# Kernel optimization log

Measured on AMD Instinct MI355X. Metric: run time of the kernel, lower is better.

The kernel has to match this reference:

```python
import jax, jax.numpy as jnp
import numpy as np

N = 20000
NEG_SLOPE = 0.2


def gatv2_layer(x, src, dst, edge_attr, Wl, bl, Wr, br, We, att, bias, H, C):
    """PyG GATv2Conv: add self-loops (edge_attr fill='mean'), gather-score-softmax-aggregate."""
    n = x.shape[0]
    E = src.shape[0]
    # --- add self loops, self-loop edge_attr = mean of incoming edge_attr per node ---
    ea_sum = jax.ops.segment_sum(edge_attr, dst, num_segments=n)
    deg = jax.ops.segment_sum(jnp.ones((E, 1), x.dtype), dst, num_segments=n)
    ea_loop = ea_sum / jnp.maximum(deg, 1.0)
    loop = jnp.arange(n)
    src_a = jnp.concatenate([src, loop])
    dst_a = jnp.concatenate([dst, loop])
    ea = jnp.concatenate([edge_attr, ea_loop], axis=0)
    # --- linear projections ---
    xl = (x @ Wl + bl).reshape(n, H, C)   # source-side features
    xr = (x @ Wr + br).reshape(n, H, C)   # target-side features
    e = (ea @ We).reshape(-1, H, C)       # edge features
    # --- per-edge GATv2 attention score ---
    m = xl[src_a] + xr[dst_a] + e                          # [E', H, C]
    s = jnp.sum(jax.nn.leaky_relu(m, NEG_SLOPE) * att, -1)  # [E', H]
    # --- softmax over incoming edges of each target node ---
    smax = jax.ops.segment_max(s, dst_a, num_segments=n)
    ex = jnp.exp(s - smax[dst_a])
    denom = jax.ops.segment_sum(ex, dst_a, num_segments=n)
    alpha = ex / (denom[dst_a] + 1e-16)                    # [E', H]
    # --- aggregate messages (alpha * x_l[src]) ---
    out = jax.ops.segment_sum(alpha[..., None] * xl[src_a], dst_a, num_segments=n)
    return out.reshape(n, H * C) + bias


def setup_inputs() -> dict:
    key = jax.random.key(0)
    ks = jax.random.split(key, 20)
    F, HID, H1, A = 128, 32, 8, 128
    E = 640000
    d = {}
    d["x"] = jax.random.normal(ks[0], (N, F), jnp.float32)
    d["edge_index"] = jax.random.randint(ks[1], (2, E), 0, N, jnp.int32).astype(jnp.int64)
    d["edge_attr"] = jax.random.normal(ks[2], (E, 1), jnp.float32)
    # layer 1 params (in=F, out=HID, heads=H1)
    d["W1l"] = jax.random.normal(ks[3], (F, H1 * HID), jnp.float32) * 0.05
    d["b1l"] = jnp.zeros((H1 * HID,), jnp.float32)
    d["W1r"] = jax.random.normal(ks[4], (F, H1 * HID), jnp.float32) * 0.05
    d["b1r"] = jnp.zeros((H1 * HID,), jnp.float32)
    d["We1"] = jax.random.normal(ks[5], (1, H1 * HID), jnp.float32) * 0.05
    d["att1"] = jax.random.normal(ks[6], (H1, HID), jnp.float32) * 0.05
    d["bias1"] = jnp.zeros((H1 * HID,), jnp.float32)
    # layer 2 params (in=H1*HID, out=A, heads=1)
    d["W2l"] = jax.random.normal(ks[7], (H1 * HID, A), jnp.float32) * 0.05
    d["b2l"] = jnp.zeros((A,), jnp.float32)
    d["W2r"] = jax.random.normal(ks[8], (H1 * HID, A), jnp.float32) * 0.05
    d["b2r"] = jnp.zeros((A,), jnp.float32)
    d["We2"] = jax.random.normal(ks[9], (1, A), jnp.float32) * 0.05
    d["att2"] = jax.random.normal(ks[10], (1, A), jnp.float32) * 0.05
    d["bias2"] = jnp.zeros((A,), jnp.float32)
    d["alpha"] = jnp.array(0.0, jnp.float32)
    return d


def reference(x, edge_index, edge_attr, W1l, b1l, W1r, b1r, We1, att1, bias1,
              W2l, b2l, W2r, b2r, We2, att2, bias2, alpha):
    src, dst = edge_index[0], edge_index[1]
    h = jax.nn.relu(gatv2_layer(x, src, dst, edge_attr, W1l, b1l, W1r, b1r,
                                We1, att1, bias1, H=8, C=32))
    h = jax.nn.relu(gatv2_layer(h, src, dst, edge_attr, W2l, b2l, W2r, b2r,
                                We2, att2, bias2, H=1, C=128))
    pooled = jnp.mean(h, axis=0, keepdims=True)  # global_mean_pool, single graph -> [1, A]
    return jax.nn.softmax(pooled, axis=1), jax.nn.sigmoid(alpha)
```

## Files before the change

### kernel.cpp

```cpp
#include <hip/hip_runtime.h>
#include <math.h>

#define NEG_SLOPE 0.2f
#define LOG2E 1.4426950408889634f

typedef __attribute__((ext_vector_type(8))) short short8;
typedef __attribute__((ext_vector_type(4))) float f32x4;
typedef __attribute__((ext_vector_type(2))) float v2f;

__device__ __forceinline__ int imin(int a, int b) { return a < b ? a : b; }

__device__ __forceinline__ unsigned int f2bf(float f) {
    unsigned int u = __float_as_uint(f);
    return (u + 0x7fffu + ((u >> 16) & 1u)) >> 16;
}
__device__ __forceinline__ float fast_exp2(float x) {
#if __has_builtin(__builtin_amdgcn_exp2f)
    return __builtin_amdgcn_exp2f(x);
#else
    return exp2f(x);
#endif
}
__device__ __forceinline__ unsigned char f2fp8(float v) {
    return (unsigned char)(__builtin_amdgcn_cvt_pk_fp8_f32(v, v, 0, false) & 0xff);
}
template <int CTRL>
__device__ __forceinline__ float dpp_add(float v) {
    int t = __builtin_amdgcn_update_dpp(0, __float_as_int(v), CTRL, 0xF, 0xF, true);
    return v + __int_as_float(t);
}
__device__ __forceinline__ v2f pk_fma(v2f a, v2f b, v2f c) {
    v2f d;
    asm("v_pk_fma_f32 %0, %1, %2, %3" : "=v"(d) : "v"(a), "v"(b), "v"(c));
    return d;
}
__device__ __forceinline__ v2f pk_add(v2f a, v2f b) {
    v2f d;
    asm("v_pk_add_f32 %0, %1, %2" : "=v"(d) : "v"(a), "v"(b));
    return d;
}

__global__ void fused_prep(const int* __restrict__ ei, const float* __restrict__ ea,
                           unsigned long long* __restrict__ hist, int E,
                           const float* __restrict__ x, unsigned short* __restrict__ xb, int nF4,
                           const float* __restrict__ W1l, const float* __restrict__ W1r,
                           const float* __restrict__ W2l, const float* __restrict__ W2r,
                           const float* __restrict__ b1l, const float* __restrict__ b1r,
                           const float* __restrict__ b2l, const float* __restrict__ b2r,
                           unsigned short* __restrict__ Wt1, unsigned short* __restrict__ Wt2,
                           float* __restrict__ b1cat, float* __restrict__ b2cat,
                           int F, int HC1, int HC2) {
    int i = blockIdx.x * blockDim.x + threadIdx.x;
    if (i < E) {
        int d = ei[E + i];
        long long fx = (long long)__float2int_rn(ea[i] * 65536.0f);
        unsigned long long v = ((unsigned long long)fx << 32) | 1ull;
        atomicAdd(&hist[(size_t)d * 8], v);
        return;
    }
    int j = i - E;
    if (j < nF4) {
        float4 v = ((const float4*)x)[j];
        uint2 r;
        r.x = f2bf(v.x) | (f2bf(v.y) << 16);
        r.y = f2bf(v.z) | (f2bf(v.w) << 16);
        ((uint2*)xb)[j] = r;
        return;
    }
    int k = j - nF4;
    int S1 = F * HC1, S2 = HC1 * HC2;
    if (k < S1) {
        int kk = k / HC1, nn = k - kk * HC1;
        Wt1[(size_t)nn * F + kk] = (unsigned short)f2bf(W1l[k]);
    } else if (k < 2 * S1) {
        int m = k - S1;
        int kk = m / HC1, nn = m - kk * HC1;
        Wt1[(size_t)(HC1 + nn) * F + kk] = (unsigned short)f2bf(W1r[m]);
    } else if (k < 2 * S1 + S2) {
        int m = k - 2 * S1;
        int kk = m / HC2, nn = m - kk * HC2;
        Wt2[(size_t)nn * HC1 + kk] = (unsigned short)f2bf(W2l[m]);
    } else if (k < 2 * S1 + 2 * S2) {
        int m = k - 2 * S1 - S2;
        int kk = m / HC2, nn = m - kk * HC2;
        Wt2[(size_t)(HC2 + nn) * HC1 + kk] = (unsigned short)f2bf(W2r[m]);
    } else if (k < 2 * S1 + 2 * S2 + 2 * HC1) {
        int m = k - 2 * S1 - 2 * S2;
        b1cat[m] = (m < HC1) ? b1l[m] : b1r[m - HC1];
    } else if (k < 2 * S1 + 2 * S2 + 2 * HC1 + 2 * HC2) {
        int m = k - 2 * S1 - 2 * S2 - 2 * HC1;
        b2cat[m] = (m < HC2) ? b2l[m] : b2r[m - HC2];
    }
}

__global__ void scan_a(const unsigned long long* __restrict__ hist, int* __restrict__ bsum, int n) {
    __shared__ int wred[4];
    int base = blockIdx.x * 1024;
    int tid = threadIdx.x;
    int s = 0;
#pragma unroll
    for (int k = 0; k < 4; ++k) {
        int i = base + tid + k * 256;
        if (i < n) s += (int)(hist[(size_t)i * 8] & 0xffffffffull);
    }
#pragma unroll
    for (int off = 32; off > 0; off >>= 1) s += __shfl_xor(s, off, 64);
    if ((tid & 63) == 0) wred[tid >> 6] = s;
    __syncthreads();
    if (tid == 0) bsum[blockIdx.x] = wred[0] + wred[1] + wred[2] + wred[3];
}

__global__ void scan_c(const unsigned long long* __restrict__ hist,
                       const int* __restrict__ bsum, int* __restrict__ row_ptr,
                       int* __restrict__ wptr_pad, float* __restrict__ ea_loop,
                       int n, int B) {
    __shared__ int wtot[4];
    __shared__ int sh_base;
    int tid = threadIdx.x;
    int wid = tid >> 6, lane = tid & 63;
    int i0 = blockIdx.x * 1024 + tid * 4;
    int dcnt[4]; float esum[4];
#pragma unroll
    for (int k = 0; k < 4; ++k) {
        if (i0 + k < n) {
            unsigned long long h = hist[(size_t)(i0 + k) * 8];
            dcnt[k] = (int)(h & 0xffffffffull);
            esum[k] = (float)((int)(h >> 32)) * (1.0f / 65536.0f);
        } else { dcnt[k] = 0; esum[k] = 0.0f; }
    }
    int tsum = dcnt[0] + dcnt[1] + dcnt[2] + dcnt[3];
    int s = tsum;
#pragma unroll
    for (int off = 1; off < 64; off <<= 1) {
        int t = __shfl_up(s, off, 64);
        if (lane >= off) s += t;
    }
    if (lane == 63) wtot[wid] = s;
    if (tid < 64) {
        int v   = (tid < B) ? bsum[tid] : 0;
        int pre = (tid < (int)blockIdx.x) ? v : 0;
        int tot = v;
#pragma unroll
        for (int off = 32; off > 0; off >>= 1) {
            pre += __shfl_xor(pre, off, 64);
            tot += __shfl_xor(tot, off, 64);
        }
        if (tid == 0) {
            sh_base = pre;
            if (blockIdx.x == 0) row_ptr[n] = tot;
        }
    }
    __syncthreads();
    int wpre = 0;
#pragma unroll
    for (int k = 0; k < 4; ++k) if (k < wid) wpre += wtot[k];
    int pre = sh_base + wpre + (s - tsum);
    if (i0 < n) {
        int4 e;
        e.x = pre;
        e.y = pre + dcnt[0];
        e.z = e.y + dcnt[1];
        e.w = e.z + dcnt[2];
        *(int4*)(row_ptr + i0) = e;
        int ev[4] = { e.x, e.y, e.z, e.w };
        float4 el;
        el.x = esum[0] / fmaxf((float)dcnt[0], 1.0f);
        el.y = esum[1] / fmaxf((float)dcnt[1], 1.0f);
        el.z = esum[2] / fmaxf((float)dcnt[2], 1.0f);
        el.w = esum[3] / fmaxf((float)dcnt[3], 1.0f);
        *(float4*)(ea_loop + i0) = el;
#pragma unroll
        for (int k = 0; k < 4; ++k) wptr_pad[(size_t)(i0 + k) * 16] = ev[k];
    }
}

__global__ void edge_scatter(const int* __restrict__ ei, const float* __restrict__ ea,
                             int* __restrict__ wptr_pad, int2* __restrict__ spk, int E) {
    int e = blockIdx.x * blockDim.x + threadIdx.x;
    if (e < E) {
        int d = ei[E + e];
        int pos = atomicAdd(&wptr_pad[(size_t)d * 16], 1);
        spk[pos] = make_int2(ei[e], __float_as_int(ea[e]));
    }
}

template <bool OUT_FP8>
__global__ void __launch_bounds__(256)
gemm_bf16(const unsigned short* __restrict__ A, const unsigned short* __restrict__ Bt,
          const float* __restrict__ bias, void* __restrict__ Cv,
          int M, int N, int K) {
    __shared__ __attribute__((aligned(16))) unsigned short As[64 * 40];
    __shared__ __attribute__((aligned(16))) unsigned short Bs[64 * 40];
    int tid  = threadIdx.x;
    int wave = tid >> 6, lane = tid & 63;
    int m0 = blockIdx.x * 64, n0 = blockIdx.y * 64;
    int row = tid >> 2, kg = (tid & 3) * 8;

    f32x4 acc[4] = {};
    for (int kk = 0; kk < K; kk += 32) {
        int gm = m0 + row;
        uint4 av;
        if (gm < M) av = *(const uint4*)(A + (size_t)gm * K + kk + kg);
        else        av = make_uint4(0, 0, 0, 0);
        *(uint4*)&As[row * 40 + kg] = av;
        uint4 bv = *(const uint4*)(Bt + (size_t)(n0 + row) * K + kk + kg);
        *(uint4*)&Bs[row * 40 + kg] = bv;
        __syncthreads();
        short8 a = *(const short8*)&As[(wave * 16 + (lane & 15)) * 40 + (lane >> 4) * 8];
#pragma unroll
        for (int g = 0; g < 4; ++g) {
            short8 b = *(const short8*)&Bs[(g * 16 + (lane & 15)) * 40 + (lane >> 4) * 8];
            acc[g] = __builtin_amdgcn_mfma_f32_16x16x32_bf16(a, b, acc[g], 0, 0, 0);
        }
        __syncthreads();
    }
#pragma unroll
    for (int g = 0; g < 4; ++g) {
        int col = n0 + g * 16 + (lane & 15);
        float bs = bias[col];
#pragma unroll
        for (int r = 0; r < 4; ++r) {
            int grow = m0 + wave * 16 + (lane >> 4) * 4 + r;
            if (grow < M) {
                float val = acc[g][r] + bs;
                if constexpr (OUT_FP8) {
                    ((unsigned char*)Cv)[(size_t)grow * N + col] = f2fp8(val);
                } else {
                    ((unsigned short*)Cv)[(size_t)grow * N + col] = (unsigned short)f2bf(val);
                }
            }
        }
    }
}

template <int NV>
__device__ __forceinline__ void unp1(unsigned int u, v2f* xf) {
    xf[0] = __builtin_amdgcn_cvt_pk_f32_fp8(u, false);
    if constexpr (NV == 4) xf[1] = __builtin_amdgcn_cvt_pk_f32_fp8(u, true);
}
template <int G>
__device__ __forceinline__ float grp_reduce(float vs) {
    vs = dpp_add<0xB1>(vs);
    if constexpr (G >= 4)  vs = dpp_add<0x4E>(vs);
    if constexpr (G >= 8)  vs = dpp_add<0x141>(vs);
    if constexpr (G >= 16) vs = dpp_add<0x140>(vs);
    if constexpr (G >= 32) {
        int t = __builtin_amdgcn_ds_swizzle(__float_as_int(vs), 0x401F);
        vs += __int_as_float(t);
    }
    if constexpr (G >= 64) vs += __shfl_xor(vs, 32, 64);
    return vs;
}

template <int HC, int STRIDE, int C, int OUT_MODE>
__global__ void __launch_bounds__(256)
gat_agg(const unsigned char* __restrict__ xlr,
        const float* __restrict__ We, const float* __restrict__ att,
        const float* __restrict__ bias,
        const int* __restrict__ row_ptr, const int2* __restrict__ spk,
        const float* __restrict__ ea_loop,
        void* __restrict__ out, int n) {
    constexpr int NV = HC / 64;
    constexpr int NG = (NV + 1) / 2;
    constexpr int G  = C / NV;
    constexpr int SHIFT = (STRIDE == 512) ? 9 : 8;
    constexpr float K23 = 2.0f / 3.0f;
    __shared__ float red[4][128];
    int wave = threadIdx.x >> 6;
    int lane = threadIdx.x & 63;
    int node = blockIdx.x * 4 + wave;
    bool active = node < n;
    if (OUT_MODE == 0 && !active) return;
    unsigned int lo = (unsigned int)lane * NV;

    float vout[NV];
#pragma unroll
    for (int j = 0; j < NV; ++j) vout[j] = 0.0f;

    if (active) {
        auto ldd = [&](unsigned int off) -> unsigned int {
            if constexpr (NV == 4) return *(const unsigned int*)(xlr + off);
            else                   return (unsigned int)(*(const unsigned short*)(xlr + off));
        };
        auto gat = [&](int s) -> unsigned int {
            return ldd(((unsigned int)s << SHIFT) + lo);
        };
        auto W = [&](int2 s) -> float { return __int_as_float(s.y); };

        v2f xr2[NG], We2[NG], att62[NG], o2[NG];
        {
            v2f tmp[NG];
            unp1<NV>(ldd(((unsigned int)node << SHIFT) + HC + lo), tmp);
#pragma unroll
            for (int g = 0; g < NG; ++g) xr2[g] = tmp[g];
        }
#pragma unroll
        for (int g = 0; g < NG; ++g) {
            We2[g]   = *(const v2f*)(We  + lo + 2 * g);
            v2f a    = *(const v2f*)(att + lo + 2 * g);
            att62[g] = a * (0.6f * LOG2E);
            o2[g]    = v2f{0.0f, 0.0f};
        }
        float l = 0.0f;

        int start = __builtin_amdgcn_readfirstlane(row_ptr[node]);
        int end   = __builtin_amdgcn_readfirstlane(row_ptr[node + 1]);
        float ea_l = ea_loop[node];

        auto process = [&](unsigned int du, float w) {
            v2f xf[NG];
            unp1<NV>(du, xf);
            v2f w2 = {w, w};
            v2f vs6 = {0.0f, 0.0f};
            float vs4 = 0.0f;
#pragma unroll
            for (int g = 0; g < NG; ++g) {
                v2f t  = pk_fma(w2, We2[g], xr2[g]);
                v2f mm = pk_add(xf[g], t);
                vs6 = pk_fma(att62[g], mm, vs6);
                vs4 = fmaf(fabsf(mm.x), att62[g].x, vs4);
                vs4 = fmaf(fabsf(mm.y), att62[g].y, vs4);
            }
            float vs = fmaf(K23, vs4, vs6.x + vs6.y);
            vs = grp_reduce<G>(vs);
            float pr = fast_exp2(vs);
            l += pr;
            v2f pr2 = {pr, pr};
#pragma unroll
            for (int g = 0; g < NG; ++g) o2[g] = pk_fma(xf[g], pr2, o2[g]);
        };

        process(ldd(((unsigned int)node << SHIFT) + lo), ea_l);

        int cnt = end - start;
        const int2* q = spk + start;

        if (cnt >= 6) {
            int2 t;
            t = q[0]; unsigned int g0 = gat(t.x); float w0 = W(t);
            t = q[1]; unsigned int g1 = gat(t.x); float w1 = W(t);
            t = q[2]; unsigned int g2 = gat(t.x); float w2 = W(t);
            t = q[3]; unsigned int g3 = gat(t.x); float w3 = W(t);
            t = q[4]; unsigned int g4 = gat(t.x); float w4 = W(t);
            t = q[5]; unsigned int g5 = gat(t.x); float w5 = W(t);
            int p = 0;
            for (; p + 12 <= cnt; p += 6) {
                process(g0, w0); t = q[p + 6];  g0 = gat(t.x); w0 = W(t);
                process(g1, w1); t = q[p + 7];  g1 = gat(t.x); w1 = W(t);
                process(g2, w2); t = q[p + 8];  g2 = gat(t.x); w2 = W(t);
                process(g3, w3); t = q[p + 9];  g3 = gat(t.x); w3 = W(t);
                process(g4, w4); t = q[p + 10]; g4 = gat(t.x); w4 = W(t);
                process(g5, w5); t = q[p + 11]; g5 = gat(t.x); w5 = W(t);
            }
            process(g0, w0); process(g1, w1); process(g2, w2);
            process(g3, w3); process(g4, w4); process(g5, w5);
            for (int k = p + 6; k < cnt; ++k) {
                t = q[k];
                process(gat(t.x), W(t));
            }
        } else {
            for (int k = 0; k < cnt; ++k) {
                int2 t = q[k];
                process(gat(t.x), W(t));
            }
        }

        float inv = 1.0f / (l + 1e-16f);
#pragma unroll
        for (int g = 0; g < NG; ++g) {
            v2f b = *(const v2f*)(bias + lo + 2 * g);
            vout[2 * g]     = fmaxf(o2[g].x * inv + b.x, 0.0f);
            vout[2 * g + 1] = fmaxf(o2[g].y * inv + b.y, 0.0f);
        }
        if constexpr (OUT_MODE == 0) {
            unsigned short* op = (unsigned short*)out + (size_t)node * HC + lo;
            if constexpr (NV == 4) {
                uint2 t;
                t.x = f2bf(vout[0]) | (f2bf(vout[1]) << 16);
                t.y = f2bf(vout[2]) | (f2bf(vout[3]) << 16);
                *(uint2*)op = t;
            } else {
                *(unsigned int*)op = f2bf(vout[0]) | (f2bf(vout[1]) << 16);
            }
        }
    }

    if constexpr (OUT_MODE == 1) {
#pragma unroll
        for (int j = 0; j < NV; ++j) red[wave][lo + j] = vout[j];
        __syncthreads();
        if (wave == 0) {
            int c = lane;
            float a = red[0][c] + red[1][c] + red[2][c] + red[3][c];
            float b = red[0][c + 64] + red[1][c + 64] + red[2][c + 64] + red[3][c + 64];
            float* pacc = (float*)out + (size_t)(blockIdx.x & 255) * 128;
            atomicAdd(&pacc[c], a);
            atomicAdd(&pacc[c + 64], b);
        }
    }
}

__global__ void __launch_bounds__(1024)
pool_final(const float* __restrict__ partial, int nb,
           const float* __restrict__ alpha_in,
           float* __restrict__ out, int n) {
    __shared__ float acc[8][128];
    __shared__ float red[4];
    int t = threadIdx.x & 127;
    int g = threadIdx.x >> 7;
    float s = 0.0f;
    for (int b = g; b < nb; b += 8) s += partial[b * 128 + t];
    acc[g][t] = s;
    __syncthreads();
    if (threadIdx.x < 128) {
        float tot = 0.0f;
#pragma unroll
        for (int k = 0; k < 8; ++k) tot += acc[k][t];
        float mean = tot / (float)n;
        float mx = mean;
#pragma unroll
        for (int off = 32; off > 0; off >>= 1) mx = fmaxf(mx, __shfl_xor(mx, off, 64));
        if ((t & 63) == 0) red[t >> 6] = mx;
        __syncthreads();
        mx = fmaxf(red[0], red[1]);
        float ex = __expf(mean - mx);
        float sm = ex;
#pragma unroll
        for (int off = 32; off > 0; off >>= 1) sm += __shfl_xor(sm, off, 64);
        if ((t & 63) == 0) red[2 + (t >> 6)] = sm;
        __syncthreads();
        sm = red[2] + red[3];
        out[t] = ex / sm;
        if (t == 0) out[128] = 1.0f / (1.0f + __expf(-alpha_in[0]));
    }
}

extern "C" void kernel_launch(void* const* d_in, const int* in_sizes, int n_in,
                              void* d_out, int out_size, void* d_ws, size_t ws_size,
                              hipStream_t stream) {
    const float* x    = (const float*)d_in[0];
    const int*   ei   = (const int*)d_in[1];
    const float* ea   = (const float*)d_in[2];
    const float* W1l  = (const float*)d_in[3];
    const float* b1l  = (const float*)d_in[4];
    const float* W1r  = (const float*)d_in[5];
    const float* b1r  = (const float*)d_in[6];
    const float* We1  = (const float*)d_in[7];
    const float* att1 = (const float*)d_in[8];
    const float* bias1= (const float*)d_in[9];
    const float* W2l  = (const float*)d_in[10];
    const float* b2l  = (const float*)d_in[11];
    const float* W2r  = (const float*)d_in[12];
    const float* b2r  = (const float*)d_in[13];
    const float* We2  = (const float*)d_in[14];
    const float* att2 = (const float*)d_in[15];
    const float* bias2= (const float*)d_in[16];
    const float* alpha= (const float*)d_in[17];
    float* out = (float*)d_out;

    const int F = 128, HC1 = 256, HC2 = 128;
    const int n = in_sizes[0] / F;
    const int E = in_sizes[1] / 2;
    const int B = (n + 1023) / 1024;

    char* ws = (char*)d_ws;
    size_t off = 0;
    auto alloc = [&](size_t bytes) { size_t p = off; off += (bytes + 255) & ~(size_t)255; return p; };

    unsigned long long* hist = (unsigned long long*)(ws + alloc((size_t)n * 8 * 8));
    int*   row_ptr = (int*)  (ws + alloc((size_t)(n + 1) * 4));
    int*   wptr    = (int*)  (ws + alloc((size_t)n * 16 * 4));
    float* ea_loop = (float*)(ws + alloc((size_t)n * 4));
    int*   bsum    = (int*)  (ws + alloc(64 * 4));
    int2*  spk     = (int2*) (ws + alloc((size_t)E * 8));
    unsigned short* xb   = (unsigned short*)(ws + alloc((size_t)n * F * 2));
    unsigned short* Wt1  = (unsigned short*)(ws + alloc((size_t)F * (2 * HC1) * 2));
    unsigned short* Wt2  = (unsigned short*)(ws + alloc((size_t)HC1 * (2 * HC2) * 2));
    float* b1cat   = (float*)(ws + alloc((size_t)2 * HC1 * 4));
    float* b2cat   = (float*)(ws + alloc((size_t)2 * HC2 * 4));
    unsigned char* xlr1 = (unsigned char*)(ws + alloc((size_t)n * 2 * HC1));
    unsigned short* h1  = (unsigned short*)(ws + alloc((size_t)n * HC1 * 2));
    float* partial = (float*)(ws + alloc((size_t)256 * 128 * 4));
    unsigned char* xlr2 = xlr1;
    const int NB_SLOTS = 256;

    (void)hipMemsetAsync(hist, 0, (size_t)n * 8 * 8, stream);
    (void)hipMemsetAsync(partial, 0, (size_t)NB_SLOTS * 128 * 4, stream);

    int tb = 256;
    {
        int nF4  = n * F / 4;
        int WTOT = 2 * F * HC1 + 2 * HC1 * HC2 + 2 * HC1 + 2 * HC2;
        int total = E + nF4 + WTOT;
        fused_prep<<<(total + tb - 1) / tb, tb, 0, stream>>>(
            ei, ea, hist, E, x, xb, nF4,
            W1l, W1r, W2l, W2r, b1l, b1r, b2l, b2r,
            Wt1, Wt2, b1cat, b2cat, F, HC1, HC2);
    }
    scan_a<<<B, 256, 0, stream>>>(hist, bsum, n);
    scan_c<<<B, 256, 0, stream>>>(hist, bsum, row_ptr, wptr, ea_loop, n, B);
    edge_scatter<<<(E + tb - 1) / tb, tb, 0, stream>>>(ei, ea, wptr, spk, E);

    {
        dim3 grid((n + 63) / 64, (2 * HC1) / 64);
        gemm_bf16<true><<<grid, 256, 0, stream>>>(xb, Wt1, b1cat, xlr1, n, 2 * HC1, F);
    }
    gat_agg<256, 512, 32, 0><<<(n + 3) / 4, 256, 0, stream>>>(
        xlr1, We1, att1, bias1, row_ptr, spk, ea_loop, h1, n);

    {
        dim3 grid((n + 63) / 64, (2 * HC2) / 64);
        gemm_bf16<true><<<grid, 256, 0, stream>>>(h1, Wt2, b2cat, xlr2, n, 2 * HC2, HC1);
    }
    gat_agg<128, 256, 128, 1><<<(n + 3) / 4, 256, 0, stream>>>(
        xlr2, We2, att2, bias2, row_ptr, spk, ea_loop, partial, n);

    pool_final<<<1, 1024, 0, stream>>>(partial, NB_SLOTS, alpha, out, n);
}
```

Measured before the change: 276.5 us.

## Load edge list cooperatively per wave and broadcast via readlane with deeper prefetch

Each wave now loads up to 64 (src, weight) edge pairs in one coalesced vector load, one per lane. It then broadcasts each pair with readlane instead of issuing per-edge uniform loads. The gather pipeline changes from a rolling 6-deep prefetch to double-buffered batches of 8 outstanding neighbour-row gathers, and the self-row load is issued earlier. This is meant to cut scalar load latency on the edge list and keep more gathers in flight, at the cost of more registers and readlane overhead.

```diff
diff --git a/kernel.cpp b/kernel.cpp
--- a/kernel.cpp
+++ b/kernel.cpp
@@ -285,7 +285,16 @@
         auto gat = [&](int s) -> unsigned int {
             return ldd(((unsigned int)s << SHIFT) + lo);
         };
-        auto W = [&](int2 s) -> float { return __int_as_float(s.y); };
+
+        int start = __builtin_amdgcn_readfirstlane(row_ptr[node]);
+        int end   = __builtin_amdgcn_readfirstlane(row_ptr[node + 1]);
+        int cnt = end - start;
+
+        int2 pv;
+        if (cnt > 0) pv = spk[imin(start + lane, end - 1)];
+
+        unsigned int selfg = ldd(((unsigned int)node << SHIFT) + lo);
+        float ea_l = ea_loop[node];
 
         v2f xr2[NG], We2[NG], att62[NG], o2[NG];
         {
@@ -302,10 +311,6 @@
             o2[g]    = v2f{0.0f, 0.0f};
         }
         float l = 0.0f;
-
-        int start = __builtin_amdgcn_readfirstlane(row_ptr[node]);
-        int end   = __builtin_amdgcn_readfirstlane(row_ptr[node + 1]);
-        float ea_l = ea_loop[node];
 
         auto process = [&](unsigned int du, float w) {
             v2f xf[NG];
@@ -329,40 +334,56 @@
 #pragma unroll
             for (int g = 0; g < NG; ++g) o2[g] = pk_fma(xf[g], pr2, o2[g]);
         };
-
-        process(ldd(((unsigned int)node << SHIFT) + lo), ea_l);
-
-        int cnt = end - start;
-        const int2* q = spk + start;
-
-        if (cnt >= 6) {
-            int2 t;
-            t = q[0]; unsigned int g0 = gat(t.x); float w0 = W(t);
-            t = q[1]; unsigned int g1 = gat(t.x); float w1 = W(t);
-            t = q[2]; unsigned int g2 = gat(t.x); float w2 = W(t);
-            t = q[3]; unsigned int g3 = gat(t.x); float w3 = W(t);
-            t = q[4]; unsigned int g4 = gat(t.x); float w4 = W(t);
-            t = q[5]; unsigned int g5 = gat(t.x); float w5 = W(t);
-            int p = 0;
-            for (; p + 12 <= cnt; p += 6) {
-                process(g0, w0); t = q[p + 6];  g0 = gat(t.x); w0 = W(t);
-                process(g1, w1); t = q[p + 7];  g1 = gat(t.x); w1 = W(t);
-                process(g2, w2); t = q[p + 8];  g2 = gat(t.x); w2 = W(t);
-                process(g3, w3); t = q[p + 9];  g3 = gat(t.x); w3 = W(t);
-                process(g4, w4); t = q[p + 10]; g4 = gat(t.x); w4 = W(t);
-                process(g5, w5); t = q[p + 11]; g5 = gat(t.x); w5 = W(t);
+        auto RLs = [&](int k) -> int { return __builtin_amdgcn_readlane(pv.x, k); };
+        auto RLw = [&](int k) -> float { return __int_as_float(__builtin_amdgcn_readlane(pv.y, k)); };
+
+        process(selfg, ea_l);
+
+        int b0 = 0;
+        while (b0 < cnt) {
+            int rem = imin(64, cnt - b0);
+            int rc = rem - 1;
+            if (rem >= 8) {
+                unsigned int a0 = gat(RLs(0)), a1 = gat(RLs(1)), a2 = gat(RLs(2)), a3 = gat(RLs(3));
+                unsigned int a4 = gat(RLs(4)), a5 = gat(RLs(5)), a6 = gat(RLs(6)), a7 = gat(RLs(7));
+                float x0 = RLw(0), x1 = RLw(1), x2 = RLw(2), x3 = RLw(3);
+                float x4 = RLw(4), x5 = RLw(5), x6 = RLw(6), x7 = RLw(7);
+                int p = 0;
+                for (; p + 16 <= rem; p += 16) {
+                    unsigned int b0r = gat(RLs(p + 8)),  b1r = gat(RLs(p + 9));
+                    unsigned int b2r = gat(RLs(p + 10)), b3r = gat(RLs(p + 11));
+                    unsigned int b4r = gat(RLs(p + 12)), b5r = gat(RLs(p + 13));
+                    unsigned int b6r = gat(RLs(p + 14)), b7r = gat(RLs(p + 15));
+                    float y0 = RLw(p + 8),  y1 = RLw(p + 9),  y2 = RLw(p + 10), y3 = RLw(p + 11);
+                    float y4 = RLw(p + 12), y5 = RLw(p + 13), y6 = RLw(p + 14), y7 = RLw(p + 15);
+                    process(a0, x0); process(a1, x1); process(a2, x2); process(a3, x3);
+                    process(a4, x4); process(a5, x5); process(a6, x6); process(a7, x7);
+                    a0 = gat(RLs(imin(p + 16, rc))); a1 = gat(RLs(imin(p + 17, rc)));
+                    a2 = gat(RLs(imin(p + 18, rc))); a3 = gat(RLs(imin(p + 19, rc)));
+                    a4 = gat(RLs(imin(p + 20, rc))); a5 = gat(RLs(imin(p + 21, rc)));
+                    a6 = gat(RLs(imin(p + 22, rc))); a7 = gat(RLs(imin(p + 23, rc)));
+                    x0 = RLw(imin(p + 16, rc)); x1 = RLw(imin(p + 17, rc));
+                    x2 = RLw(imin(p + 18, rc)); x3 = RLw(imin(p + 19, rc));
+                    x4 = RLw(imin(p + 20, rc)); x5 = RLw(imin(p + 21, rc));
+                    x6 = RLw(imin(p + 22, rc)); x7 = RLw(imin(p + 23, rc));
+                    process(b0r, y0); process(b1r, y1); process(b2r, y2); process(b3r, y3);
+                    process(b4r, y4); process(b5r, y5); process(b6r, y6); process(b7r, y7);
+                }
+                int r = rem - p;
+                if (r > 0) process(a0, x0);
+                if (r > 1) process(a1, x1);
+                if (r > 2) process(a2, x2);
+                if (r > 3) process(a3, x3);
+                if (r > 4) process(a4, x4);
+                if (r > 5) process(a5, x5);
+                if (r > 6) process(a6, x6);
+                if (r > 7) process(a7, x7);
+                for (int k = p + 8; k < rem; ++k) process(gat(RLs(k)), RLw(k));
+            } else {
+                for (int k = 0; k < rem; ++k) process(gat(RLs(k)), RLw(k));
             }
-            process(g0, w0); process(g1, w1); process(g2, w2);
-            process(g3, w3); process(g4, w4); process(g5, w5);
-            for (int k = p + 6; k < cnt; ++k) {
-                t = q[k];
-                process(gat(t.x), W(t));
-            }
-        } else {
-            for (int k = 0; k < cnt; ++k) {
-                int2 t = q[k];
-                process(gat(t.x), W(t));
-            }
+            b0 += 64;
+            if (b0 < cnt) pv = spk[imin(start + b0 + lane, end - 1)];
         }
 
         float inv = 1.0f / (l + 1e-16f);
```

After: 282.6 us. +2.2%, slower.
